# Kernel optimization log

Hardware: AMD Instinct MI355X
Metric: run time of the kernel (lower is better)

The kernel has to match this reference:

```python
import jax, jax.numpy as jnp
import numpy as np

N, E, R, D = 50000, 640000, 200, 128  # nodes, edges, relations, feat dim (in_feat==out_feat)
EPS = 1e-5  # LayerNorm eps
NEG_SLOPE = 0.01  # F.leaky_relu default

def _xavier(k, shape):
    gain = np.sqrt(2.0)  # calculate_gain('relu')
    std = gain * np.sqrt(2.0 / (shape[0] + shape[1]))
    a = np.sqrt(3.0) * std
    return jax.random.uniform(k, shape, jnp.float32, -a, a)

def setup_inputs() -> dict:
    key = jax.random.key(0)
    ks = jax.random.split(key, 10)
    return {
        "node": jax.random.normal(ks[0], (N, D), jnp.float32),
        "rel": jax.random.normal(ks[1], (R, D), jnp.float32),
        "norm": jax.random.uniform(ks[2], (N, 1), jnp.float32),
        "w_triplet": _xavier(ks[3], (3 * D, D)),
        "w_quad": _xavier(ks[4], (D, D)),
        "loop_weight": _xavier(ks[5], (D, D)),
        "evolve_loop_weight": _xavier(ks[6], (D, D)),
        "src": jax.random.randint(ks[7], (E,), 0, N),
        "dst": jax.random.randint(ks[8], (E,), 0, N),
        "etype": jax.random.randint(ks[9], (E,), 0, R),
    }

def reference(node, rel, norm, w_triplet, w_quad, loop_weight, evolve_loop_weight, src, dst, etype):
    # triplet = cat([h_src, rel_emb, h_dst], 1) @ w_triplet, computed blockwise
    # to avoid materializing the [E, 3D] concat.
    W_s, W_r, W_d = w_triplet[:D], w_triplet[D:2 * D], w_triplet[2 * D:]
    triplet = node[src] @ W_s + rel[etype] @ W_r + node[dst] @ W_d  # [E, D]
    # 'fre' not in edata -> sro_fre is zeros; a_triplet = triplet @ w_quad
    a = jax.nn.leaky_relu(triplet @ w_quad, negative_slope=NEG_SLOPE)  # [E, D]
    # edge_softmax: softmax over incoming edges per destination node, per feature
    a_max = jax.ops.segment_max(a, dst, num_segments=N)
    a_max = jnp.where(jnp.isfinite(a_max), a_max, 0.0)  # empty segments -> -inf
    ex = jnp.exp(a - a_max[dst])
    denom = jax.ops.segment_sum(ex, dst, num_segments=N)
    att = ex / denom[dst]
    # weighted scatter-sum aggregation, then apply_func: h * norm
    h = jax.ops.segment_sum(att * triplet, dst, num_segments=N) * norm  # [N, D]
    # self-loop: evolve_loop_weight for in-degree-0 nodes, loop_weight otherwise
    indeg = jax.ops.segment_sum(jnp.ones((E,), jnp.float32), dst, num_segments=N)
    loop = jnp.where((indeg > 0)[:, None], node @ loop_weight, node @ evolve_loop_weight)
    out = h + loop
    # LayerNorm(elementwise_affine=False)
    mu = jnp.mean(out, axis=-1, keepdims=True)
    var = jnp.var(out, axis=-1, keepdims=True)
    return (out - mu) * jax.lax.rsqrt(var + EPS)
```

## Files before the change

### kernel.cpp

```cpp
#include <hip/hip_runtime.h>
#include <hip/hip_bf16.h>

#define D 128
#define LOG2E 1.4426950408889634f

typedef __attribute__((ext_vector_type(8))) short bf16x8;
typedef __attribute__((ext_vector_type(4))) float f32x4;
typedef __attribute__((ext_vector_type(2))) float f32x2;
typedef __attribute__((ext_vector_type(2))) unsigned u32x2;
typedef __attribute__((ext_vector_type(4))) unsigned u32x4;

__device__ __forceinline__ unsigned short f2bf_bits(float f) {
    union { __hip_bfloat16 h; unsigned short u; } c;
    c.h = __float2bfloat16(f);
    return c.u;
}
__device__ __forceinline__ float bfbits2f(unsigned short u) {
    return __uint_as_float(((unsigned)u) << 16);
}
__device__ __forceinline__ float ldf(const void* p, size_t i, int f32) {
    return f32 ? ((const float*)p)[i] : bfbits2f(((const unsigned short*)p)[i]);
}
__device__ __forceinline__ f32x2 unpk2(unsigned u) {
    f32x2 r;
    r.x = __uint_as_float(u << 16);
    r.y = __uint_as_float(u & 0xFFFF0000u);
    return r;
}
__device__ __forceinline__ f32x2 shx32(f32x2 v) {
    f32x2 r;
    r.x = __shfl_xor(v.x, 32);
    r.y = __shfl_xor(v.y, 32);
    return r;
}
__device__ __forceinline__ f32x2 pk_add(f32x2 a, f32x2 b) {
    f32x2 d;
    asm("v_pk_add_f32 %0, %1, %2" : "=v"(d) : "v"(a), "v"(b));
    return d;
}
__device__ __forceinline__ f32x2 pk_mul(f32x2 a, f32x2 b) {
    f32x2 d;
    asm("v_pk_mul_f32 %0, %1, %2" : "=v"(d) : "v"(a), "v"(b));
    return d;
}
__device__ __forceinline__ f32x2 pk_fma(f32x2 a, f32x2 b, f32x2 c) {
    f32x2 d;
    asm("v_pk_fma_f32 %0, %1, %2, %3" : "=v"(d) : "v"(a), "v"(b), "v"(c));
    return d;
}
__device__ __forceinline__ float fexp2(float x) {
    float r;
    asm("v_exp_f32 %0, %1" : "=v"(r) : "v"(x));
    return r;
}

__global__ __launch_bounds__(256) void prep_kernel(
    const void* __restrict__ node, const void* __restrict__ wtrip,
    const void* __restrict__ wquad, const void* __restrict__ loopW,
    const void* __restrict__ evoW, unsigned short* __restrict__ wT,
    int* __restrict__ cnt, int* __restrict__ rank,
    const int* __restrict__ dst, int* __restrict__ flag, int E) {
    __shared__ int sflag;
    int tid = threadIdx.x;
    int bad = 0;
    if (tid < 64) {
        for (int j = 0; j < 4; j++) {
            float v = bfbits2f(((const unsigned short*)node)[tid + 64 * j]);
            if (!(fabsf(v) < 1e4f)) bad = 1;
        }
    }
    unsigned long long m = __ballot(bad);
    if (tid == 0) sflag = (m != 0ull) ? 1 : 0;
    __syncthreads();
    int f32 = sflag;
    int bx = blockIdx.x;
    if (bx == 0 && tid == 0) *flag = f32;

    if (bx < 192) {
        int unit = bx * 2 + (tid >> 7);
        int k = unit & 127, mjob = unit >> 7;
        int t = tid & 127;
        float acc = 0.f;
        for (int j = 0; j < D; j++)
            acc += ldf(wtrip, (size_t)mjob * D * D + (size_t)k * D + j, f32) *
                   ldf(wquad, (size_t)j * D + t, f32);
        const int jmap0 = (mjob == 0) ? 0 : (mjob == 1 ? 6 : 2);
        wT[(size_t)jmap0 * D * D + (size_t)t * D + k] = f2bf_bits(acc);
    } else if (bx < 272) {
        int u = bx - 192;
        int jr = u >> 4, seg = u & 15;
        const void* srcp; size_t base; int j;
        switch (jr) {
            case 0: srcp = wtrip; base = 0;             j = 1; break;
            case 1: srcp = wtrip; base = 2 * D * D;     j = 3; break;
            case 2: srcp = loopW; base = 0;             j = 4; break;
            case 3: srcp = evoW;  base = 0;             j = 5; break;
            default: srcp = wtrip; base = (size_t)D * D; j = 7; break;
        }
        for (int c = tid; c < 1024; c += 256) {
            int idx = seg * 1024 + c;
            int n = idx >> 7, k = idx & 127;
            unsigned short b = f32 ? f2bf_bits(((const float*)srcp)[base + (size_t)k * D + n])
                                   : ((const unsigned short*)srcp)[base + (size_t)k * D + n];
            wT[(size_t)j * D * D + (size_t)n * D + k] = b;
        }
    } else {
        int e = (bx - 272) * 256 + tid;
        if (e < E) rank[e] = atomicAdd(&cnt[dst[e]], 1);
    }
}

__global__ void scan_block(const int* __restrict__ cnt, int* __restrict__ offs,
                           int* __restrict__ part, int N) {
    __shared__ int sh[256];
    int tid = threadIdx.x;
    int i = blockIdx.x * 256 + tid;
    int v = (i < N) ? cnt[i] : 0;
    sh[tid] = v;
    __syncthreads();
    for (int o = 1; o < 256; o <<= 1) {
        int t = (tid >= o) ? sh[tid - o] : 0;
        __syncthreads();
        sh[tid] += t;
        __syncthreads();
    }
    if (i < N) offs[i] = sh[tid] - v;
    if (tid == 255) part[blockIdx.x] = sh[255];
}

__global__ void scan_fix(int* __restrict__ offs, const int* __restrict__ part,
                         int N, int E) {
    __shared__ int sh[256];
    int tid = threadIdx.x, b = blockIdx.x;
    sh[tid] = (tid < b) ? part[tid] : 0;
    __syncthreads();
    for (int o = 128; o; o >>= 1) {
        if (tid < o) sh[tid] += sh[tid + o];
        __syncthreads();
    }
    int carry = sh[0];
    int i = b * 256 + tid;
    if (i < N) offs[i] += carry;
    if (b == 0 && tid == 0) offs[N] = E;
}

__global__ __launch_bounds__(512) void gemm_kernel(
    const void* __restrict__ node, const void* __restrict__ rel,
    const unsigned short* __restrict__ wT, const int* __restrict__ cnt,
    unsigned* __restrict__ nodeST, unsigned* __restrict__ nodeDT,
    unsigned* __restrict__ relRT, unsigned* __restrict__ loopSel,
    const int* __restrict__ flag, int N, int R, int nodeBlocks,
    const int* __restrict__ src, const int* __restrict__ dst,
    const int* __restrict__ et, const int* __restrict__ offs,
    const int* __restrict__ rank, unsigned* __restrict__ ePack, int E) {
    __shared__ __align__(16) unsigned short Wt[D][D + 8];

    int bx = blockIdx.x, by = blockIdx.y;
    int tid = threadIdx.y * 64 + threadIdx.x;
    int isRel = 0, jp;
    if (bx >= nodeBlocks) {
        if (by == 1) {
            int e = (bx - nodeBlocks) * 512 + tid;
            if (e < E) {
                int d = dst[e];
                ePack[offs[d] + rank[e]] = (unsigned)src[e] | ((unsigned)et[e] << 20);
            }
            return;
        }
        if (by != 0 || bx - nodeBlocks >= (R + 127) / 128) return;
        isRel = 1;
        jp = 3;
    } else {
        jp = by;
    }

    int f32 = *flag;
    int rows = isRel ? R : N;
    int row0 = (isRel ? bx - nodeBlocks : bx) * 128;
    const void* A = isRel ? rel : node;

    int lane = threadIdx.x, wv = threadIdx.y;
    int l16 = lane & 15, quad = lane >> 4;
    int ar = row0 + wv * 16 + l16;
    int ar_c = ar < rows ? ar : rows - 1;

    int qIdx, tIdx;
    unsigned* O = nullptr;
    switch (jp) {
        case 0: qIdx = 0; tIdx = 1; O = nodeST; break;
        case 1: qIdx = 2; tIdx = 3; O = nodeDT; break;
        case 2: qIdx = 4; tIdx = 5; break;
        default: qIdx = 6; tIdx = 7; O = relRT; break;
    }

    bf16x8 af[4];
#pragma unroll
    for (int kk = 0; kk < 4; kk++) {
        int k = kk * 32 + quad * 8;
        if (f32) {
            const float* Af = (const float*)A + (size_t)ar_c * D + k;
            float4 x0 = *(const float4*)(Af);
            float4 x1 = *(const float4*)(Af + 4);
            af[kk][0] = (short)f2bf_bits(x0.x);
            af[kk][1] = (short)f2bf_bits(x0.y);
            af[kk][2] = (short)f2bf_bits(x0.z);
            af[kk][3] = (short)f2bf_bits(x0.w);
            af[kk][4] = (short)f2bf_bits(x1.x);
            af[kk][5] = (short)f2bf_bits(x1.y);
            af[kk][6] = (short)f2bf_bits(x1.z);
            af[kk][7] = (short)f2bf_bits(x1.w);
        } else {
            af[kk] = *(const bf16x8*)((const unsigned short*)A + (size_t)ar_c * D + k);
        }
    }

    const unsigned short* gQ = wT + (size_t)qIdx * D * D;
    const unsigned short* gT = wT + (size_t)tIdx * D * D;

    bf16x8 wreg[4], wreg2[4];
#pragma unroll
    for (int i = 0; i < 4; i++) {
        int c = tid + i * 512;
        wreg[i] = *(const bf16x8*)(gQ + (c >> 4) * 128 + (c & 15) * 8);
    }

    f32x4 accQ[8], accT[8];
#pragma unroll
    for (int i = 0; i < 8; i++) {
        accQ[i] = (f32x4){0.f, 0.f, 0.f, 0.f};
        accT[i] = (f32x4){0.f, 0.f, 0.f, 0.f};
    }

    for (int pass = 0; pass < 2; pass++) {
#pragma unroll
        for (int i = 0; i < 4; i++) {
            int c = tid + i * 512;
            *(bf16x8*)(&Wt[c >> 4][(c & 15) * 8]) = wreg[i];
        }
        if (pass == 0) {
#pragma unroll
            for (int i = 0; i < 4; i++) {
                int c = tid + i * 512;
                wreg2[i] = *(const bf16x8*)(gT + (c >> 4) * 128 + (c & 15) * 8);
            }
        }
        __syncthreads();
        f32x4* acc = pass ? accT : accQ;
#pragma unroll
        for (int kk = 0; kk < 4; kk++) {
#pragma unroll
            for (int nt = 0; nt < 8; nt++) {
                bf16x8 bfr = *(const bf16x8*)(&Wt[nt * 16 + l16][kk * 32 + quad * 8]);
                acc[nt] = __builtin_amdgcn_mfma_f32_16x16x32_bf16(af[kk], bfr, acc[nt], 0, 0, 0);
            }
        }
        __syncthreads();
#pragma unroll
        for (int i = 0; i < 4; i++) wreg[i] = wreg2[i];
    }

    int cr0 = row0 + wv * 16 + quad * 4;
    int odd = l16 & 1;
    if (jp != 2) {
#pragma unroll
        for (int r = 0; r < 4; r++) {
            int cr = cr0 + r;
#pragma unroll
            for (int nt = 0; nt < 8; nt++) {
                float vQ = accQ[nt][r] * LOG2E;
                float vT = accT[nt][r];
                float oQ = __shfl_xor(vQ, 1);
                float oT = __shfl_xor(vT, 1);
                unsigned w;
                if (!odd) w = (unsigned)f2bf_bits(vQ) | ((unsigned)f2bf_bits(oQ) << 16);
                else      w = (unsigned)f2bf_bits(oT) | ((unsigned)f2bf_bits(vT) << 16);
                if (cr < rows) O[(size_t)cr * 128 + nt * 16 + l16] = w;
            }
        }
    } else {
#pragma unroll
        for (int r = 0; r < 4; r++) {
            int cr = cr0 + r;
            int deg = (cr < rows) ? cnt[cr] : 0;
#pragma unroll
            for (int nt = 0; nt < 8; nt++) {
                float vL = accQ[nt][r], vE = accT[nt][r];
                float oL = __shfl_xor(vL, 1);
                float oE = __shfl_xor(vE, 1);
                unsigned wl, we;
                if (!odd) {
                    wl = (unsigned)f2bf_bits(vL) | ((unsigned)f2bf_bits(oL) << 16);
                    we = (unsigned)f2bf_bits(vE) | ((unsigned)f2bf_bits(oE) << 16);
                } else {
                    wl = (unsigned)f2bf_bits(oL) | ((unsigned)f2bf_bits(vL) << 16);
                    we = (unsigned)f2bf_bits(oE) | ((unsigned)f2bf_bits(vE) << 16);
                }
                if (cr < rows && !odd)
                    loopSel[(size_t)cr * 64 + nt * 8 + (l16 >> 1)] = (deg > 0) ? wl : we;
            }
        }
    }
}

__global__ __launch_bounds__(256) void agg_kernel(
    const int* __restrict__ offs, const unsigned* __restrict__ ePack,
    const unsigned* __restrict__ ST, const unsigned* __restrict__ RT,
    const unsigned* __restrict__ DT, const unsigned* __restrict__ loopSel,
    const void* __restrict__ normv, void* __restrict__ out,
    const int* __restrict__ flag, int N) {
    int n = blockIdx.x * 4 + threadIdx.y;
    if (n >= N) return;
    int f32 = *flag;
    int lane = threadIdx.x;
    int half = lane >> 5, sl = lane & 31;
    int start = offs[n], end = offs[n + 1];
    int deg = end - start;

    u32x4 ud = *(const u32x4*)(DT + (size_t)n * 128 + sl * 4);
    f32x2 qd01 = unpk2(ud.x), td01 = unpk2(ud.y);
    f32x2 qd23 = unpk2(ud.z), td23 = unpk2(ud.w);
    u32x2 ul = *(const u32x2*)(loopSel + (size_t)n * 64 + sl * 2);
    f32x2 acc01 = unpk2(ul.x), acc23 = unpk2(ul.y);

    const char* STb = (const char*)ST;
    const char* RTb = (const char*)RT;
    unsigned laneoff = (unsigned)(sl * 16);

    f32x2 den01 = {0.f, 0.f}, den23 = {0.f, 0.f};
    f32x2 h01 = {0.f, 0.f}, h23 = {0.f, 0.f};
    const f32x2 ns2 = {0.01f, 0.01f};

#define GLOAD(PK, US, UR)                                                   \
    u32x4 US = *(const u32x4*)(STb + ((((PK) & 0xFFFFFu) << 9) + laneoff)); \
    u32x4 UR = *(const u32x4*)(RTb + ((((PK) >> 20) << 9) + laneoff));

#define EMATH(US, UR)                                                       \
    {                                                                       \
        f32x2 q01 = pk_add(pk_add(unpk2(US.x), unpk2(UR.x)), qd01);         \
        f32x2 q23 = pk_add(pk_add(unpk2(US.z), unpk2(UR.z)), qd23);         \
        f32x2 s01 = pk_mul(q01, ns2);                                       \
        f32x2 s23 = pk_mul(q23, ns2);                                       \
        f32x2 ex01, ex23;                                                   \
        ex01.x = fexp2(fmaxf(q01.x, s01.x));                                \
        ex01.y = fexp2(fmaxf(q01.y, s01.y));                                \
        ex23.x = fexp2(fmaxf(q23.x, s23.x));                                \
        ex23.y = fexp2(fmaxf(q23.y, s23.y));                                \
        den01 = pk_add(den01, ex01); den23 = pk_add(den23, ex23);           \
        f32x2 t01 = pk_add(pk_add(unpk2(US.y), unpk2(UR.y)), td01);         \
        f32x2 t23 = pk_add(pk_add(unpk2(US.w), unpk2(UR.w)), td23);         \
        h01 = pk_fma(ex01, t01, h01);                                       \
        h23 = pk_fma(ex23, t23, h23);                                       \
    }

#define EMATHV(US, UR, VM)                                                  \
    {                                                                       \
        f32x2 q01 = pk_add(pk_add(unpk2(US.x), unpk2(UR.x)), qd01);         \
        f32x2 q23 = pk_add(pk_add(unpk2(US.z), unpk2(UR.z)), qd23);         \
        f32x2 s01 = pk_mul(q01, ns2);                                       \
        f32x2 s23 = pk_mul(q23, ns2);                                       \
        f32x2 ex01, ex23;                                                   \
        ex01.x = fexp2(fmaxf(q01.x, s01.x)) * (VM);                         \
        ex01.y = fexp2(fmaxf(q01.y, s01.y)) * (VM);                         \
        ex23.x = fexp2(fmaxf(q23.x, s23.x)) * (VM);                         \
        ex23.y = fexp2(fmaxf(q23.y, s23.y)) * (VM);                         \
        den01 = pk_add(den01, ex01); den23 = pk_add(den23, ex23);           \
        f32x2 t01 = pk_add(pk_add(unpk2(US.y), unpk2(UR.y)), td01);         \
        f32x2 t23 = pk_add(pk_add(unpk2(US.w), unpk2(UR.w)), td23);         \
        h01 = pk_fma(ex01, t01, h01);                                       \
        h23 = pk_fma(ex23, t23, h23);                                       \
    }

    int e = start;
    for (; e + 3 < end; e += 4) {
        unsigned pA = ePack[e + half];
        unsigned pB = ePack[e + 2 + half];
        GLOAD(pA, usA, urA)
        GLOAD(pB, usB, urB)
        EMATH(usA, urA)
        EMATH(usB, urB)
    }
    for (; e < end; e += 2) {
        int eh = e + half;
        int valid = eh < end;
        unsigned pT = ePack[valid ? eh : end - 1];
        GLOAD(pT, usT, urT)
        EMATHV(usT, urT, valid ? 1.0f : 0.0f)
    }
#undef GLOAD
#undef EMATH
#undef EMATHV

    den01 = pk_add(den01, shx32(den01)); den23 = pk_add(den23, shx32(den23));
    h01 = pk_add(h01, shx32(h01));       h23 = pk_add(h23, shx32(h23));

    f32x2 x01, x23;
    if (deg > 0) {
        float nrm = ldf(normv, n, f32);
        x01 = h01 / den01 * nrm + acc01;
        x23 = h23 / den23 * nrm + acc23;
    } else {
        x01 = acc01;
        x23 = acc23;
    }

    float s = (x01.x + x01.y) + (x23.x + x23.y);
    float ss = (x01.x * x01.x + x01.y * x01.y) + (x23.x * x23.x + x23.y * x23.y);
#pragma unroll
    for (int o = 16; o; o >>= 1) {
        s += __shfl_xor(s, o);
        ss += __shfl_xor(ss, o);
    }
    float mu = s * (1.f / 128.f);
    float var = ss * (1.f / 128.f) - mu * mu;
    float rstd = rsqrtf(var + 1e-5f);
    f32x2 y01 = (x01 - mu) * rstd;
    f32x2 y23 = (x23 - mu) * rstd;

    if (half == 0) {
        if (f32) {
            float4 o4 = make_float4(y01.x, y01.y, y23.x, y23.y);
            ((float4*)out)[(size_t)n * 32 + sl] = o4;
        } else {
            u32x2 ow;
            ow.x = (unsigned)f2bf_bits(y01.x) | ((unsigned)f2bf_bits(y01.y) << 16);
            ow.y = (unsigned)f2bf_bits(y23.x) | ((unsigned)f2bf_bits(y23.y) << 16);
            *(u32x2*)((unsigned*)out + (size_t)n * 64 + sl * 2) = ow;
        }
    }
}

extern "C" void kernel_launch(void* const* d_in, const int* in_sizes, int n_in,
                              void* d_out, int out_size, void* d_ws, size_t ws_size,
                              hipStream_t stream) {
    const void* node = d_in[0];
    const void* rel = d_in[1];
    const void* normv = d_in[2];
    const void* wtrip = d_in[3];
    const void* wquad = d_in[4];
    const void* loopW = d_in[5];
    const void* evoW = d_in[6];
    const int* src = (const int*)d_in[7];
    const int* dst = (const int*)d_in[8];
    const int* et = (const int*)d_in[9];

    int N = in_sizes[0] / D;
    int R = in_sizes[1] / D;
    int E = in_sizes[7];
    int nb = (N + 255) / 256;
    int nodeBlocks = (N + 127) / 128;
    int relBlocks = (R + 127) / 128;
    int scatBlocks = (E + 511) / 512;

    char* p = (char*)d_ws;
    auto alloc = [&](size_t bytes) -> void* {
        void* r = (void*)p;
        p += (bytes + 255) & ~(size_t)255;
        return r;
    };
    unsigned* nodeST = (unsigned*)alloc((size_t)N * 128 * 4);
    unsigned* nodeDT = (unsigned*)alloc((size_t)N * 128 * 4);
    unsigned* relRT = (unsigned*)alloc((size_t)R * 128 * 4);
    unsigned* loopSel = (unsigned*)alloc((size_t)N * 64 * 4);
    unsigned short* wT = (unsigned short*)alloc((size_t)8 * D * D * 2);
    int* cnt = (int*)alloc((size_t)N * 4);
    int* offs = (int*)alloc((size_t)(N + 1) * 4);
    int* part = (int*)alloc((size_t)(nb + 1) * 4);
    int* rank = (int*)alloc((size_t)E * 4);
    unsigned* ePack = (unsigned*)alloc((size_t)E * 4);
    int* flag = (int*)alloc(4);

    hipMemsetAsync(cnt, 0, (size_t)N * 4, stream);
    prep_kernel<<<272 + (E + 255) / 256, 256, 0, stream>>>(
        node, wtrip, wquad, loopW, evoW, wT, cnt, rank, dst, flag, E);
    scan_block<<<nb, 256, 0, stream>>>(cnt, offs, part, N);
    scan_fix<<<nb, 256, 0, stream>>>(offs, part, N, E);
    int xext = nodeBlocks + (scatBlocks > relBlocks ? scatBlocks : relBlocks);
    gemm_kernel<<<dim3(xext, 3), dim3(64, 8), 0, stream>>>(
        node, rel, wT, cnt, nodeST, nodeDT, relRT, loopSel, flag, N, R, nodeBlocks,
        src, dst, et, offs, rank, ePack, E);
    agg_kernel<<<(N + 3) / 4, dim3(64, 4), 0, stream>>>(
        offs, ePack, nodeST, relRT, nodeDT, loopSel, normv, d_out, flag, N);
}
```

Baseline: 233.6 us.

## Read GEMM weights directly from global memory and pre-shift edge pack offsets

The GEMM kernel no longer stages the transposed weight matrices through shared memory with block barriers. Each lane now loads its MFMA B-fragments straight from global memory, relying on L1/L2 caching, which removes the LDS writes and two __syncthreads per pass. Separately, the packed edge record grows from one 32-bit word to two, storing src and etype already shifted into byte offsets. This drops the mask and shift work from the aggregation inner loop, but doubles the bytes read per edge. Uncoalesced global B-fragment loads may cost more than the LDS traffic they replace.

```diff
diff --git a/kernel.cpp b/kernel.cpp
--- a/kernel.cpp
+++ b/kernel.cpp
@@ -152,9 +152,7 @@
     const int* __restrict__ flag, int N, int R, int nodeBlocks,
     const int* __restrict__ src, const int* __restrict__ dst,
     const int* __restrict__ et, const int* __restrict__ offs,
-    const int* __restrict__ rank, unsigned* __restrict__ ePack, int E) {
-    __shared__ __align__(16) unsigned short Wt[D][D + 8];
-
+    const int* __restrict__ rank, u32x2* __restrict__ ePack, int E) {
     int bx = blockIdx.x, by = blockIdx.y;
     int tid = threadIdx.y * 64 + threadIdx.x;
     int isRel = 0, jp;
@@ -163,7 +161,10 @@
             int e = (bx - nodeBlocks) * 512 + tid;
             if (e < E) {
                 int d = dst[e];
-                ePack[offs[d] + rank[e]] = (unsigned)src[e] | ((unsigned)et[e] << 20);
+                u32x2 pk;
+                pk.x = ((unsigned)src[e]) << 9;
+                pk.y = ((unsigned)et[e]) << 9;
+                ePack[offs[d] + rank[e]] = pk;
             }
             return;
         }
@@ -214,15 +215,8 @@
         }
     }
 
-    const unsigned short* gQ = wT + (size_t)qIdx * D * D;
-    const unsigned short* gT = wT + (size_t)tIdx * D * D;
-
-    bf16x8 wreg[4], wreg2[4];
-#pragma unroll
-    for (int i = 0; i < 4; i++) {
-        int c = tid + i * 512;
-        wreg[i] = *(const bf16x8*)(gQ + (c >> 4) * 128 + (c & 15) * 8);
-    }
+    const unsigned short* gQ = wT + (size_t)qIdx * D * D + (size_t)l16 * D + quad * 8;
+    const unsigned short* gT = wT + (size_t)tIdx * D * D + (size_t)l16 * D + quad * 8;
 
     f32x4 accQ[8], accT[8];
 #pragma unroll
@@ -231,32 +225,21 @@
         accT[i] = (f32x4){0.f, 0.f, 0.f, 0.f};
     }
 
-    for (int pass = 0; pass < 2; pass++) {
-#pragma unroll
-        for (int i = 0; i < 4; i++) {
-            int c = tid + i * 512;
-            *(bf16x8*)(&Wt[c >> 4][(c & 15) * 8]) = wreg[i];
-        }
-        if (pass == 0) {
-#pragma unroll
-            for (int i = 0; i < 4; i++) {
-                int c = tid + i * 512;
-                wreg2[i] = *(const bf16x8*)(gT + (c >> 4) * 128 + (c & 15) * 8);
-            }
-        }
-        __syncthreads();
-        f32x4* acc = pass ? accT : accQ;
+#pragma unroll
+    for (int nt = 0; nt < 8; nt++) {
 #pragma unroll
         for (int kk = 0; kk < 4; kk++) {
-#pragma unroll
-            for (int nt = 0; nt < 8; nt++) {
-                bf16x8 bfr = *(const bf16x8*)(&Wt[nt * 16 + l16][kk * 32 + quad * 8]);
-                acc[nt] = __builtin_amdgcn_mfma_f32_16x16x32_bf16(af[kk], bfr, acc[nt], 0, 0, 0);
-            }
-        }
-        __syncthreads();
-#pragma unroll
-        for (int i = 0; i < 4; i++) wreg[i] = wreg2[i];
+            bf16x8 bq = *(const bf16x8*)(gQ + nt * 16 * D + kk * 32);
+            accQ[nt] = __builtin_amdgcn_mfma_f32_16x16x32_bf16(af[kk], bq, accQ[nt], 0, 0, 0);
+        }
+    }
+#pragma unroll
+    for (int nt = 0; nt < 8; nt++) {
+#pragma unroll
+        for (int kk = 0; kk < 4; kk++) {
+            bf16x8 bt = *(const bf16x8*)(gT + nt * 16 * D + kk * 32);
+            accT[nt] = __builtin_amdgcn_mfma_f32_16x16x32_bf16(af[kk], bt, accT[nt], 0, 0, 0);
+        }
     }
 
     int cr0 = row0 + wv * 16 + quad * 4;
@@ -303,7 +286,7 @@
 }
 
 __global__ __launch_bounds__(256) void agg_kernel(
-    const int* __restrict__ offs, const unsigned* __restrict__ ePack,
+    const int* __restrict__ offs, const u32x2* __restrict__ ePack,
     const unsigned* __restrict__ ST, const unsigned* __restrict__ RT,
     const unsigned* __restrict__ DT, const unsigned* __restrict__ loopSel,
     const void* __restrict__ normv, void* __restrict__ out,
@@ -331,8 +314,8 @@
     const f32x2 ns2 = {0.01f, 0.01f};
 
 #define GLOAD(PK, US, UR)                                                   \
-    u32x4 US = *(const u32x4*)(STb + ((((PK) & 0xFFFFFu) << 9) + laneoff)); \
-    u32x4 UR = *(const u32x4*)(RTb + ((((PK) >> 20) << 9) + laneoff));
+    u32x4 US = *(const u32x4*)(STb + (size_t)((PK).x + laneoff));           \
+    u32x4 UR = *(const u32x4*)(RTb + (size_t)((PK).y + laneoff));
 
 #define EMATH(US, UR)                                                       \
     {                                                                       \
@@ -372,8 +355,8 @@
 
     int e = start;
     for (; e + 3 < end; e += 4) {
-        unsigned pA = ePack[e + half];
-        unsigned pB = ePack[e + 2 + half];
+        u32x2 pA = ePack[e + half];
+        u32x2 pB = ePack[e + 2 + half];
         GLOAD(pA, usA, urA)
         GLOAD(pB, usB, urB)
         EMATH(usA, urA)
@@ -382,7 +365,7 @@
     for (; e < end; e += 2) {
         int eh = e + half;
         int valid = eh < end;
-        unsigned pT = ePack[valid ? eh : end - 1];
+        u32x2 pT = ePack[valid ? eh : end - 1];
         GLOAD(pT, usT, urT)
         EMATHV(usT, urT, valid ? 1.0f : 0.0f)
     }
@@ -466,7 +449,7 @@
     int* offs = (int*)alloc((size_t)(N + 1) * 4);
     int* part = (int*)alloc((size_t)(nb + 1) * 4);
     int* rank = (int*)alloc((size_t)E * 4);
-    unsigned* ePack = (unsigned*)alloc((size_t)E * 4);
+    u32x2* ePack = (u32x2*)alloc((size_t)E * 8);
     int* flag = (int*)alloc(4);
 
     hipMemsetAsync(cnt, 0, (size_t)N * 4, stream);
```

Result: slower. 284.2 us (+21.7%).
